# Kernel tuning notes

Measured on AMD Instinct MI355X. Metric: run time of the kernel, lower is better.

Reference implementation:

```python
import jax, jax.numpy as jnp
import numpy as np
from jax import lax

T, IN, H, B = 256, 2048, 2048, 8
K_INIT = 4.0

def setup_inputs() -> dict:
    key = jax.random.key(0)
    k1, k2, k3, k4, k5, k6 = jax.random.split(key, 6)
    k = 1.0 / np.sqrt(H)
    # simplex-init alphas: off-diagonal -K, diagonal log(1-(B-1)exp(-K)), plus small noise
    base = jnp.full((B, B), -K_INIT) + jnp.eye(B) * (np.log(1.0 - (B - 1) * np.exp(-K_INIT)) + K_INIT)
    alphas = base + 0.01 * jax.random.normal(k1, (B, B))
    return {
        "x": jax.random.normal(k2, (T, IN), dtype=jnp.float32),            # sentence of word vectors
        "W": jax.random.uniform(k3, (B, H, H), minval=-k, maxval=k),       # B recurrent basis matrices
        "alphas": alphas.astype(jnp.float32),                               # [B, B] mixing logits
        "bias": jax.random.uniform(k4, (H,), minval=-k, maxval=k),
        "v": jnp.eye(H, IN, dtype=jnp.float32),                             # input projection (init = eye)
        "fc_w": jax.random.uniform(k5, (H, H), minval=-k, maxval=k),
        "fc_b": jax.random.uniform(k6, (H,), minval=-k, maxval=k),
        "alpha_int": 0,
    }

def reference(x, W, alphas, bias, v, fc_w, fc_b, alpha_int):
    # normalise_alpha == softmax over the selected alpha row (simplex=True)
    alpha = jax.nn.softmax(alphas[alpha_int])                 # [B]
    u = jnp.einsum('b,bij->ij', alpha, W)                     # mixed recurrent weight [H, H]
    igates = x @ v.T                                          # all input gates at once [T, H]

    def step(h, ig):                                          # Elman cell: h = tanh(v@w + u@h + bias)
        h = jnp.tanh(ig + u @ h + bias)
        return h, None

    h0 = jnp.zeros((H,), dtype=x.dtype)
    h, _ = lax.scan(step, h0, igates)                         # sequential over T words
    out = jax.nn.sigmoid(h @ fc_w.T + fc_b)                   # fc(hidden.t()) then sigmoid
    return out[None, :]                                       # [1, H]
```

## Files before the change

kernel.cpp:

```cpp
#include <hip/hip_runtime.h>
#include <math.h>

#define NBLK    64
#define NTHR    512
#define HDIM    2048
#define TSTEPS  256
#define BBASIS  8
#define RPB     32
#define RPW     4
#define TTILE   8

typedef float f32x4 __attribute__((ext_vector_type(4)));

__device__ inline void store_coherent_f4(float* p, f32x4 v) {
    asm volatile("global_store_dwordx4 %0, %1, off sc0 sc1"
                 :: "v"(p), "v"(v) : "memory");
}

__device__ inline f32x4 load_coherent_f4(const float* p) {
    f32x4 a;
    asm volatile("global_load_dwordx4 %0, %1, off sc0 sc1\n\t"
                 "s_waitcnt vmcnt(0)"
                 : "=&v"(a) : "v"(p) : "memory");
    return a;
}

__global__ __launch_bounds__(NTHR, 1)
void elman_scan_kernel(const float* __restrict__ x,
                       const float* __restrict__ W,
                       const float* __restrict__ alphas,
                       const float* __restrict__ bias,
                       const float* __restrict__ v,
                       const float* __restrict__ fc_w,
                       const float* __restrict__ fc_b,
                       const int*   __restrict__ alpha_int,
                       float*       __restrict__ out,
                       float*       __restrict__ hbuf)
{
    const int tid  = threadIdx.x;
    const int bid  = blockIdx.x;
    const int wave = tid >> 6;
    const int lane = tid & 63;
    const int r0   = bid * RPB + wave * RPW;

    __shared__ __align__(16) float x_tile[TTILE][HDIM];
    __shared__ __align__(16) float ig_lds[TSTEPS][RPB];
    __shared__ __align__(16) float h_lds[2][HDIM];
    __shared__ __align__(16) float hstage[RPB];

    const int ai = alpha_int[0];
    float a[BBASIS];
    float mx = -1e30f;
    #pragma unroll
    for (int b = 0; b < BBASIS; ++b) { a[b] = alphas[ai * BBASIS + b]; mx = fmaxf(mx, a[b]); }
    float ssum = 0.f;
    #pragma unroll
    for (int b = 0; b < BBASIS; ++b) { a[b] = expf(a[b] - mx); ssum += a[b]; }
    const float inv_s = 1.f / ssum;

    {
        float vr[RPW][8][4];
        #pragma unroll
        for (int q = 0; q < RPW; ++q) {
            const f32x4* vrow = (const f32x4*)(v + (size_t)(r0 + q) * HDIM);
            #pragma unroll
            for (int k = 0; k < 8; ++k) {
                f32x4 t4 = vrow[lane + 64 * k];
                vr[q][k][0] = t4.x; vr[q][k][1] = t4.y; vr[q][k][2] = t4.z; vr[q][k][3] = t4.w;
            }
        }
        for (int tb = 0; tb < TSTEPS; tb += TTILE) {
            #pragma unroll
            for (int j = 0; j < TTILE; ++j)
                *(f32x4*)&x_tile[j][4 * tid] =
                    *(const f32x4*)&x[(size_t)(tb + j) * HDIM + 4 * tid];
            __syncthreads();
            #pragma unroll
            for (int j = 0; j < TTILE; ++j) {
                float acc0 = 0.f, acc1 = 0.f, acc2 = 0.f, acc3 = 0.f;
                #pragma unroll
                for (int k = 0; k < 8; ++k) {
                    const f32x4 x4 = ((const f32x4*)x_tile[j])[lane + 64 * k];
                    acc0 += vr[0][k][0]*x4.x + vr[0][k][1]*x4.y + vr[0][k][2]*x4.z + vr[0][k][3]*x4.w;
                    acc1 += vr[1][k][0]*x4.x + vr[1][k][1]*x4.y + vr[1][k][2]*x4.z + vr[1][k][3]*x4.w;
                    acc2 += vr[2][k][0]*x4.x + vr[2][k][1]*x4.y + vr[2][k][2]*x4.z + vr[2][k][3]*x4.w;
                    acc3 += vr[3][k][0]*x4.x + vr[3][k][1]*x4.y + vr[3][k][2]*x4.z + vr[3][k][3]*x4.w;
                }
                #pragma unroll
                for (int off = 32; off > 0; off >>= 1) {
                    acc0 += __shfl_xor(acc0, off, 64);
                    acc1 += __shfl_xor(acc1, off, 64);
                    acc2 += __shfl_xor(acc2, off, 64);
                    acc3 += __shfl_xor(acc3, off, 64);
                }
                if (lane == 0) {
                    f32x4 ig4; ig4.x = acc0; ig4.y = acc1; ig4.z = acc2; ig4.w = acc3;
                    *(f32x4*)&ig_lds[tb + j][wave * RPW] = ig4;
                }
            }
            __syncthreads();
        }
    }

    float u_reg[RPW][8][4];
    #pragma unroll
    for (int q = 0; q < RPW; ++q)
        #pragma unroll
        for (int k = 0; k < 8; ++k)
            #pragma unroll
            for (int i = 0; i < 4; ++i) u_reg[q][k][i] = 0.f;

    for (int b = 0; b < BBASIS; ++b) {
        const float ab = a[b] * inv_s;
        #pragma unroll
        for (int q = 0; q < RPW; ++q) {
            const f32x4* wrow = (const f32x4*)(W + ((size_t)b * HDIM + (size_t)(r0 + q)) * HDIM);
            #pragma unroll
            for (int k = 0; k < 8; ++k) {
                f32x4 w4 = wrow[lane + 64 * k];
                u_reg[q][k][0] += ab * w4.x;
                u_reg[q][k][1] += ab * w4.y;
                u_reg[q][k][2] += ab * w4.z;
                u_reg[q][k][3] += ab * w4.w;
            }
        }
    }
    float bias4[RPW];
    #pragma unroll
    for (int q = 0; q < RPW; ++q) bias4[q] = bias[r0 + q];

    for (int i = tid; i < HDIM; i += NTHR) h_lds[0][i] = 0.f;
    __syncthreads();

    int cur = 0;
    for (int t = 0; t < TSTEPS; ++t) {
        float acc0 = 0.f, acc1 = 0.f, acc2 = 0.f, acc3 = 0.f;
        #pragma unroll
        for (int k = 0; k < 8; ++k) {
            const f32x4 h4 = ((const f32x4*)h_lds[cur])[lane + 64 * k];
            acc0 += u_reg[0][k][0]*h4.x + u_reg[0][k][1]*h4.y + u_reg[0][k][2]*h4.z + u_reg[0][k][3]*h4.w;
            acc1 += u_reg[1][k][0]*h4.x + u_reg[1][k][1]*h4.y + u_reg[1][k][2]*h4.z + u_reg[1][k][3]*h4.w;
            acc2 += u_reg[2][k][0]*h4.x + u_reg[2][k][1]*h4.y + u_reg[2][k][2]*h4.z + u_reg[2][k][3]*h4.w;
            acc3 += u_reg[3][k][0]*h4.x + u_reg[3][k][1]*h4.y + u_reg[3][k][2]*h4.z + u_reg[3][k][3]*h4.w;
        }
        #pragma unroll
        for (int off = 32; off > 0; off >>= 1) {
            acc0 += __shfl_xor(acc0, off, 64);
            acc1 += __shfl_xor(acc1, off, 64);
            acc2 += __shfl_xor(acc2, off, 64);
            acc3 += __shfl_xor(acc3, off, 64);
        }
        if (lane == 0) {
            const f32x4 ig4 = *(const f32x4*)&ig_lds[t][wave * RPW];
            f32x4 hv;
            hv.x = tanhf(acc0 + ig4.x + bias4[0]);
            hv.y = tanhf(acc1 + ig4.y + bias4[1]);
            hv.z = tanhf(acc2 + ig4.z + bias4[2]);
            hv.w = tanhf(acc3 + ig4.w + bias4[3]);
            *(f32x4*)&hstage[wave * RPW] = hv;
        }
        __syncthreads();

        float* hg = hbuf + (size_t)(t + 1) * HDIM;
        if (wave == 0 && lane < 8) {
            f32x4 hv = *(const f32x4*)&hstage[lane * 4];
            store_coherent_f4(hg + bid * RPB + lane * 4, hv);
        }

        const float* pp = hg + 4 * tid;
        f32x4 hq = load_coherent_f4(pp);
        const unsigned s = 0xFFFFFFFFu;
        while ((__float_as_uint(hq.x) == s) | (__float_as_uint(hq.y) == s) |
               (__float_as_uint(hq.z) == s) | (__float_as_uint(hq.w) == s)) {
            __builtin_amdgcn_s_sleep(2);
            hq = load_coherent_f4(pp);
        }
        const int nxt = cur ^ 1;
        *(f32x4*)&h_lds[nxt][4 * tid] = hq;
        __syncthreads();
        cur = nxt;
    }

    {
        float acc0 = 0.f, acc1 = 0.f, acc2 = 0.f, acc3 = 0.f;
        const f32x4* f0 = (const f32x4*)(fc_w + (size_t)(r0 + 0) * HDIM);
        const f32x4* f1 = (const f32x4*)(fc_w + (size_t)(r0 + 1) * HDIM);
        const f32x4* f2 = (const f32x4*)(fc_w + (size_t)(r0 + 2) * HDIM);
        const f32x4* f3 = (const f32x4*)(fc_w + (size_t)(r0 + 3) * HDIM);
        #pragma unroll
        for (int k = 0; k < 8; ++k) {
            const f32x4 h4 = ((const f32x4*)h_lds[cur])[lane + 64 * k];
            f32x4 w0 = f0[lane + 64 * k];
            f32x4 w1 = f1[lane + 64 * k];
            f32x4 w2 = f2[lane + 64 * k];
            f32x4 w3 = f3[lane + 64 * k];
            acc0 += w0.x*h4.x + w0.y*h4.y + w0.z*h4.z + w0.w*h4.w;
            acc1 += w1.x*h4.x + w1.y*h4.y + w1.z*h4.z + w1.w*h4.w;
            acc2 += w2.x*h4.x + w2.y*h4.y + w2.z*h4.z + w2.w*h4.w;
            acc3 += w3.x*h4.x + w3.y*h4.y + w3.z*h4.z + w3.w*h4.w;
        }
        #pragma unroll
        for (int off = 32; off > 0; off >>= 1) {
            acc0 += __shfl_xor(acc0, off, 64);
            acc1 += __shfl_xor(acc1, off, 64);
            acc2 += __shfl_xor(acc2, off, 64);
            acc3 += __shfl_xor(acc3, off, 64);
        }
        if (lane == 0) {
            f32x4 o4;
            o4.x = 1.f / (1.f + expf(-(acc0 + fc_b[r0 + 0])));
            o4.y = 1.f / (1.f + expf(-(acc1 + fc_b[r0 + 1])));
            o4.z = 1.f / (1.f + expf(-(acc2 + fc_b[r0 + 2])));
            o4.w = 1.f / (1.f + expf(-(acc3 + fc_b[r0 + 3])));
            *(f32x4*)&out[r0] = o4;
        }
    }
}

extern "C" void kernel_launch(void* const* d_in, const int* in_sizes, int n_in,
                              void* d_out, int out_size, void* d_ws, size_t ws_size,
                              hipStream_t stream)
{
    const float* x      = (const float*)d_in[0];
    const float* W      = (const float*)d_in[1];
    const float* alphas = (const float*)d_in[2];
    const float* bias   = (const float*)d_in[3];
    const float* v      = (const float*)d_in[4];
    const float* fc_w   = (const float*)d_in[5];
    const float* fc_b   = (const float*)d_in[6];
    const int*   ai     = (const int*)d_in[7];
    float* out = (float*)d_out;

    float* hbuf = (float*)d_ws;
    const size_t hbuf_bytes = (size_t)(TSTEPS + 1) * HDIM * sizeof(float);

    hipMemsetAsync(d_ws, 0xFF, hbuf_bytes, stream);

    elman_scan_kernel<<<NBLK, NTHR, 0, stream>>>(x, W, alphas, bias, v, fc_w, fc_b,
                                                 ai, out, hbuf);
}
```

Baseline: 1.043 ms.

## Split prep (mixed weights, input gates) into wide kernel before persistent scan

Moves the basis mixing of W and the x@v.T input-gate projection into a separate prep kernel launched on 256 blocks, writing u and igates to workspace. The persistent 64-block scan kernel then only loads them. This spreads the setup work across more CUs than the 64 used by the scan. The scan step also drops the LDS staging and extra barrier: each wave's lane 0 stores its 4 h values directly, and the spin sleep is shortened. The cost is an extra kernel launch and a global round-trip for u and igates. The original single kernel remains as a fallback when the workspace is too small.

```diff
diff --git a/kernel.cpp b/kernel.cpp
--- a/kernel.cpp
+++ b/kernel.cpp
@@ -1,14 +1,9 @@
 #include <hip/hip_runtime.h>
 #include <math.h>
 
-#define NBLK    64
-#define NTHR    512
 #define HDIM    2048
 #define TSTEPS  256
 #define BBASIS  8
-#define RPB     32
-#define RPW     4
-#define TTILE   8
 
 typedef float f32x4 __attribute__((ext_vector_type(4)));
 
@@ -16,7 +11,6 @@
     asm volatile("global_store_dwordx4 %0, %1, off sc0 sc1"
                  :: "v"(p), "v"(v) : "memory");
 }
-
 __device__ inline f32x4 load_coherent_f4(const float* p) {
     f32x4 a;
     asm volatile("global_load_dwordx4 %0, %1, off sc0 sc1\n\t"
@@ -25,28 +19,22 @@
     return a;
 }
 
-__global__ __launch_bounds__(NTHR, 1)
-void elman_scan_kernel(const float* __restrict__ x,
-                       const float* __restrict__ W,
-                       const float* __restrict__ alphas,
-                       const float* __restrict__ bias,
-                       const float* __restrict__ v,
-                       const float* __restrict__ fc_w,
-                       const float* __restrict__ fc_b,
-                       const int*   __restrict__ alpha_int,
-                       float*       __restrict__ out,
-                       float*       __restrict__ hbuf)
+__global__ __launch_bounds__(256, 1)
+void prep_kernel(const float* __restrict__ x,
+                 const float* __restrict__ W,
+                 const float* __restrict__ alphas,
+                 const float* __restrict__ v,
+                 const int*   __restrict__ alpha_int,
+                 float*       __restrict__ u_g,
+                 float*       __restrict__ ig_g)
 {
     const int tid  = threadIdx.x;
     const int bid  = blockIdx.x;
     const int wave = tid >> 6;
     const int lane = tid & 63;
-    const int r0   = bid * RPB + wave * RPW;
-
-    __shared__ __align__(16) float x_tile[TTILE][HDIM];
-    __shared__ __align__(16) float ig_lds[TSTEPS][RPB];
-    __shared__ __align__(16) float h_lds[2][HDIM];
-    __shared__ __align__(16) float hstage[RPB];
+    const int r0   = bid * 8 + wave * 2;
+
+    __shared__ __align__(16) float x_tile[8][HDIM];
 
     const int ai = alpha_int[0];
     float a[BBASIS];
@@ -59,9 +47,46 @@
     const float inv_s = 1.f / ssum;
 
     {
-        float vr[RPW][8][4];
-        #pragma unroll
-        for (int q = 0; q < RPW; ++q) {
+        float acc[2][8][4];
+        #pragma unroll
+        for (int q = 0; q < 2; ++q)
+            #pragma unroll
+            for (int k = 0; k < 8; ++k)
+                #pragma unroll
+                for (int i = 0; i < 4; ++i) acc[q][k][i] = 0.f;
+
+        for (int b = 0; b < BBASIS; ++b) {
+            const float ab = a[b] * inv_s;
+            #pragma unroll
+            for (int q = 0; q < 2; ++q) {
+                const f32x4* wrow = (const f32x4*)(W + ((size_t)b * HDIM + (size_t)(r0 + q)) * HDIM);
+                #pragma unroll
+                for (int k = 0; k < 8; ++k) {
+                    f32x4 w4 = wrow[lane + 64 * k];
+                    acc[q][k][0] += ab * w4.x;
+                    acc[q][k][1] += ab * w4.y;
+                    acc[q][k][2] += ab * w4.z;
+                    acc[q][k][3] += ab * w4.w;
+                }
+            }
+        }
+        #pragma unroll
+        for (int q = 0; q < 2; ++q) {
+            f32x4* urow = (f32x4*)(u_g + (size_t)(r0 + q) * HDIM);
+            #pragma unroll
+            for (int k = 0; k < 8; ++k) {
+                f32x4 w4;
+                w4.x = acc[q][k][0]; w4.y = acc[q][k][1];
+                w4.z = acc[q][k][2]; w4.w = acc[q][k][3];
+                urow[lane + 64 * k] = w4;
+            }
+        }
+    }
+
+    {
+        float vr[2][8][4];
+        #pragma unroll
+        for (int q = 0; q < 2; ++q) {
             const f32x4* vrow = (const f32x4*)(v + (size_t)(r0 + q) * HDIM);
             #pragma unroll
             for (int k = 0; k < 8; ++k) {
@@ -69,14 +94,214 @@
                 vr[q][k][0] = t4.x; vr[q][k][1] = t4.y; vr[q][k][2] = t4.z; vr[q][k][3] = t4.w;
             }
         }
-        for (int tb = 0; tb < TSTEPS; tb += TTILE) {
-            #pragma unroll
-            for (int j = 0; j < TTILE; ++j)
+        for (int tb = 0; tb < TSTEPS; tb += 8) {
+            #pragma unroll
+            for (int j = 0; j < 8; ++j) {
+                const f32x4* xt4 = (const f32x4*)(x + (size_t)(tb + j) * HDIM);
+                #pragma unroll
+                for (int c = 0; c < 2; ++c)
+                    ((f32x4*)x_tile[j])[tid + 256 * c] = xt4[tid + 256 * c];
+            }
+            __syncthreads();
+            #pragma unroll
+            for (int j = 0; j < 8; ++j) {
+                float acc0 = 0.f, acc1 = 0.f;
+                #pragma unroll
+                for (int k = 0; k < 8; ++k) {
+                    const f32x4 x4 = ((const f32x4*)x_tile[j])[lane + 64 * k];
+                    acc0 += vr[0][k][0]*x4.x + vr[0][k][1]*x4.y + vr[0][k][2]*x4.z + vr[0][k][3]*x4.w;
+                    acc1 += vr[1][k][0]*x4.x + vr[1][k][1]*x4.y + vr[1][k][2]*x4.z + vr[1][k][3]*x4.w;
+                }
+                #pragma unroll
+                for (int off = 32; off > 0; off >>= 1) {
+                    acc0 += __shfl_xor(acc0, off, 64);
+                    acc1 += __shfl_xor(acc1, off, 64);
+                }
+                if (lane == 0)
+                    *(float2*)&ig_g[(size_t)(tb + j) * HDIM + r0] = make_float2(acc0, acc1);
+            }
+            __syncthreads();
+        }
+    }
+}
+
+__global__ __launch_bounds__(512, 1)
+void scan_kernel(const float* __restrict__ bias,
+                 const float* __restrict__ fc_w,
+                 const float* __restrict__ fc_b,
+                 float*       __restrict__ out,
+                 const float* __restrict__ u_g,
+                 const float* __restrict__ ig_g,
+                 float*       __restrict__ hbuf)
+{
+    const int tid  = threadIdx.x;
+    const int bid  = blockIdx.x;
+    const int wave = tid >> 6;
+    const int lane = tid & 63;
+    const int r0   = bid * 32 + wave * 4;
+
+    __shared__ __align__(16) float h_lds[2][HDIM];
+    __shared__ __align__(16) float ig_lds[TSTEPS][32];
+
+    #pragma unroll
+    for (int i = 0; i < 4; ++i) {
+        const int c  = tid + 512 * i;
+        const int t  = c >> 3;
+        const int ch = c & 7;
+        f32x4 g = *(const f32x4*)&ig_g[(size_t)t * HDIM + bid * 32 + ch * 4];
+        *(f32x4*)&ig_lds[t][ch * 4] = g;
+    }
+
+    float u_reg[4][8][4];
+    #pragma unroll
+    for (int q = 0; q < 4; ++q) {
+        const f32x4* urow = (const f32x4*)(u_g + (size_t)(r0 + q) * HDIM);
+        #pragma unroll
+        for (int k = 0; k < 8; ++k) {
+            f32x4 w4 = urow[lane + 64 * k];
+            u_reg[q][k][0] = w4.x; u_reg[q][k][1] = w4.y;
+            u_reg[q][k][2] = w4.z; u_reg[q][k][3] = w4.w;
+        }
+    }
+    float bias4[4];
+    #pragma unroll
+    for (int q = 0; q < 4; ++q) bias4[q] = bias[r0 + q];
+
+    h_lds[0][tid]        = 0.f;
+    h_lds[0][tid + 512]  = 0.f;
+    h_lds[0][tid + 1024] = 0.f;
+    h_lds[0][tid + 1536] = 0.f;
+    __syncthreads();
+
+    int cur = 0;
+    for (int t = 0; t < TSTEPS; ++t) {
+        float acc0 = 0.f, acc1 = 0.f, acc2 = 0.f, acc3 = 0.f;
+        #pragma unroll
+        for (int k = 0; k < 8; ++k) {
+            const f32x4 h4 = ((const f32x4*)h_lds[cur])[lane + 64 * k];
+            acc0 += u_reg[0][k][0]*h4.x + u_reg[0][k][1]*h4.y + u_reg[0][k][2]*h4.z + u_reg[0][k][3]*h4.w;
+            acc1 += u_reg[1][k][0]*h4.x + u_reg[1][k][1]*h4.y + u_reg[1][k][2]*h4.z + u_reg[1][k][3]*h4.w;
+            acc2 += u_reg[2][k][0]*h4.x + u_reg[2][k][1]*h4.y + u_reg[2][k][2]*h4.z + u_reg[2][k][3]*h4.w;
+            acc3 += u_reg[3][k][0]*h4.x + u_reg[3][k][1]*h4.y + u_reg[3][k][2]*h4.z + u_reg[3][k][3]*h4.w;
+        }
+        #pragma unroll
+        for (int off = 32; off > 0; off >>= 1) {
+            acc0 += __shfl_xor(acc0, off, 64);
+            acc1 += __shfl_xor(acc1, off, 64);
+            acc2 += __shfl_xor(acc2, off, 64);
+            acc3 += __shfl_xor(acc3, off, 64);
+        }
+        float* hg = hbuf + (size_t)(t + 1) * HDIM;
+        if (lane == 0) {
+            const f32x4 ig4 = *(const f32x4*)&ig_lds[t][wave * 4];
+            f32x4 hv;
+            hv.x = tanhf(acc0 + ig4.x + bias4[0]);
+            hv.y = tanhf(acc1 + ig4.y + bias4[1]);
+            hv.z = tanhf(acc2 + ig4.z + bias4[2]);
+            hv.w = tanhf(acc3 + ig4.w + bias4[3]);
+            store_coherent_f4(hg + r0, hv);
+        }
+        const float* pp = hg + 4 * tid;
+        f32x4 hq = load_coherent_f4(pp);
+        const unsigned s = 0xFFFFFFFFu;
+        while ((__float_as_uint(hq.x) == s) | (__float_as_uint(hq.y) == s) |
+               (__float_as_uint(hq.z) == s) | (__float_as_uint(hq.w) == s)) {
+            __builtin_amdgcn_s_sleep(1);
+            hq = load_coherent_f4(pp);
+        }
+        const int nxt = cur ^ 1;
+        *(f32x4*)&h_lds[nxt][4 * tid] = hq;
+        __syncthreads();
+        cur = nxt;
+    }
+
+    {
+        float acc0 = 0.f, acc1 = 0.f, acc2 = 0.f, acc3 = 0.f;
+        const f32x4* f0 = (const f32x4*)(fc_w + (size_t)(r0 + 0) * HDIM);
+        const f32x4* f1 = (const f32x4*)(fc_w + (size_t)(r0 + 1) * HDIM);
+        const f32x4* f2 = (const f32x4*)(fc_w + (size_t)(r0 + 2) * HDIM);
+        const f32x4* f3 = (const f32x4*)(fc_w + (size_t)(r0 + 3) * HDIM);
+        #pragma unroll
+        for (int k = 0; k < 8; ++k) {
+            const f32x4 h4 = ((const f32x4*)h_lds[cur])[lane + 64 * k];
+            f32x4 w0 = f0[lane + 64 * k];
+            f32x4 w1 = f1[lane + 64 * k];
+            f32x4 w2 = f2[lane + 64 * k];
+            f32x4 w3 = f3[lane + 64 * k];
+            acc0 += w0.x*h4.x + w0.y*h4.y + w0.z*h4.z + w0.w*h4.w;
+            acc1 += w1.x*h4.x + w1.y*h4.y + w1.z*h4.z + w1.w*h4.w;
+            acc2 += w2.x*h4.x + w2.y*h4.y + w2.z*h4.z + w2.w*h4.w;
+            acc3 += w3.x*h4.x + w3.y*h4.y + w3.z*h4.z + w3.w*h4.w;
+        }
+        #pragma unroll
+        for (int off = 32; off > 0; off >>= 1) {
+            acc0 += __shfl_xor(acc0, off, 64);
+            acc1 += __shfl_xor(acc1, off, 64);
+            acc2 += __shfl_xor(acc2, off, 64);
+            acc3 += __shfl_xor(acc3, off, 64);
+        }
+        if (lane == 0) {
+            f32x4 o4;
+            o4.x = 1.f / (1.f + expf(-(acc0 + fc_b[r0 + 0])));
+            o4.y = 1.f / (1.f + expf(-(acc1 + fc_b[r0 + 1])));
+            o4.z = 1.f / (1.f + expf(-(acc2 + fc_b[r0 + 2])));
+            o4.w = 1.f / (1.f + expf(-(acc3 + fc_b[r0 + 3])));
+            *(f32x4*)&out[r0] = o4;
+        }
+    }
+}
+
+__global__ __launch_bounds__(512, 1)
+void elman_scan_self(const float* __restrict__ x,
+                     const float* __restrict__ W,
+                     const float* __restrict__ alphas,
+                     const float* __restrict__ bias,
+                     const float* __restrict__ v,
+                     const float* __restrict__ fc_w,
+                     const float* __restrict__ fc_b,
+                     const int*   __restrict__ alpha_int,
+                     float*       __restrict__ out,
+                     float*       __restrict__ hbuf)
+{
+    const int tid  = threadIdx.x;
+    const int bid  = blockIdx.x;
+    const int wave = tid >> 6;
+    const int lane = tid & 63;
+    const int r0   = bid * 32 + wave * 4;
+
+    __shared__ __align__(16) float x_tile[8][HDIM];
+    __shared__ __align__(16) float ig_lds[TSTEPS][32];
+    __shared__ __align__(16) float h_lds[2][HDIM];
+
+    const int ai = alpha_int[0];
+    float a[BBASIS];
+    float mx = -1e30f;
+    #pragma unroll
+    for (int b = 0; b < BBASIS; ++b) { a[b] = alphas[ai * BBASIS + b]; mx = fmaxf(mx, a[b]); }
+    float ssum = 0.f;
+    #pragma unroll
+    for (int b = 0; b < BBASIS; ++b) { a[b] = expf(a[b] - mx); ssum += a[b]; }
+    const float inv_s = 1.f / ssum;
+
+    {
+        float vr[4][8][4];
+        #pragma unroll
+        for (int q = 0; q < 4; ++q) {
+            const f32x4* vrow = (const f32x4*)(v + (size_t)(r0 + q) * HDIM);
+            #pragma unroll
+            for (int k = 0; k < 8; ++k) {
+                f32x4 t4 = vrow[lane + 64 * k];
+                vr[q][k][0] = t4.x; vr[q][k][1] = t4.y; vr[q][k][2] = t4.z; vr[q][k][3] = t4.w;
+            }
+        }
+        for (int tb = 0; tb < TSTEPS; tb += 8) {
+            #pragma unroll
+            for (int j = 0; j < 8; ++j)
                 *(f32x4*)&x_tile[j][4 * tid] =
                     *(const f32x4*)&x[(size_t)(tb + j) * HDIM + 4 * tid];
             __syncthreads();
             #pragma unroll
-            for (int j = 0; j < TTILE; ++j) {
+            for (int j = 0; j < 8; ++j) {
                 float acc0 = 0.f, acc1 = 0.f, acc2 = 0.f, acc3 = 0.f;
                 #pragma unroll
                 for (int k = 0; k < 8; ++k) {
@@ -95,16 +320,16 @@
                 }
                 if (lane == 0) {
                     f32x4 ig4; ig4.x = acc0; ig4.y = acc1; ig4.z = acc2; ig4.w = acc3;
-                    *(f32x4*)&ig_lds[tb + j][wave * RPW] = ig4;
+                    *(f32x4*)&ig_lds[tb + j][wave * 4] = ig4;
                 }
             }
             __syncthreads();
         }
     }
 
-    float u_reg[RPW][8][4];
-    #pragma unroll
-    for (int q = 0; q < RPW; ++q)
+    float u_reg[4][8][4];
+    #pragma unroll
+    for (int q = 0; q < 4; ++q)
         #pragma unroll
         for (int k = 0; k < 8; ++k)
             #pragma unroll
@@ -113,7 +338,7 @@
     for (int b = 0; b < BBASIS; ++b) {
         const float ab = a[b] * inv_s;
         #pragma unroll
-        for (int q = 0; q < RPW; ++q) {
+        for (int q = 0; q < 4; ++q) {
             const f32x4* wrow = (const f32x4*)(W + ((size_t)b * HDIM + (size_t)(r0 + q)) * HDIM);
             #pragma unroll
             for (int k = 0; k < 8; ++k) {
@@ -125,11 +350,12 @@
             }
         }
     }
-    float bias4[RPW];
-    #pragma unroll
-    for (int q = 0; q < RPW; ++q) bias4[q] = bias[r0 + q];
-
-    for (int i = tid; i < HDIM; i += NTHR) h_lds[0][i] = 0.f;
+    float bias4[4];
+    #pragma unroll
+    for (int q = 0; q < 4; ++q) bias4[q] = bias[r0 + q];
+
+    h_lds[0][tid] = 0.f; h_lds[0][tid + 512] = 0.f;
+    h_lds[0][tid + 1024] = 0.f; h_lds[0][tid + 1536] = 0.f;
     __syncthreads();
 
     int cur = 0;
@@ -150,29 +376,22 @@
             acc2 += __shfl_xor(acc2, off, 64);
             acc3 += __shfl_xor(acc3, off, 64);
         }
+        float* hg = hbuf + (size_t)(t + 1) * HDIM;
         if (lane == 0) {
-            const f32x4 ig4 = *(const f32x4*)&ig_lds[t][wave * RPW];
+            const f32x4 ig4 = *(const f32x4*)&ig_lds[t][wave * 4];
             f32x4 hv;
             hv.x = tanhf(acc0 + ig4.x + bias4[0]);
             hv.y = tanhf(acc1 + ig4.y + bias4[1]);
             hv.z = tanhf(acc2 + ig4.z + bias4[2]);
             hv.w = tanhf(acc3 + ig4.w + bias4[3]);
-            *(f32x4*)&hstage[wave * RPW] = hv;
-        }
-        __syncthreads();
-
-        float* hg = hbuf + (size_t)(t + 1) * HDIM;
-        if (wave == 0 && lane < 8) {
-            f32x4 hv = *(const f32x4*)&hstage[lane * 4];
-            store_coherent_f4(hg + bid * RPB + lane * 4, hv);
-        }
-
+            store_coherent_f4(hg + r0, hv);
+        }
         const float* pp = hg + 4 * tid;
         f32x4 hq = load_coherent_f4(pp);
         const unsigned s = 0xFFFFFFFFu;
         while ((__float_as_uint(hq.x) == s) | (__float_as_uint(hq.y) == s) |
                (__float_as_uint(hq.z) == s) | (__float_as_uint(hq.w) == s)) {
-            __builtin_amdgcn_s_sleep(2);
+            __builtin_amdgcn_s_sleep(1);
             hq = load_coherent_f4(pp);
         }
         const int nxt = cur ^ 1;
@@ -231,11 +450,24 @@
     const int*   ai     = (const int*)d_in[7];
     float* out = (float*)d_out;
 
+    const size_t HB_BYTES = (size_t)(TSTEPS + 1) * HDIM * sizeof(float);
+    const size_t IG_OFF   = 0x210000;
+    const size_t IG_BYTES = (size_t)TSTEPS * HDIM * sizeof(float);
+    const size_t U_OFF    = IG_OFF + 0x210000;
+    const size_t U_BYTES  = (size_t)HDIM * HDIM * sizeof(float);
+    const size_t NEED     = U_OFF + U_BYTES;
+
     float* hbuf = (float*)d_ws;
-    const size_t hbuf_bytes = (size_t)(TSTEPS + 1) * HDIM * sizeof(float);
-
-    hipMemsetAsync(d_ws, 0xFF, hbuf_bytes, stream);
-
-    elman_scan_kernel<<<NBLK, NTHR, 0, stream>>>(x, W, alphas, bias, v, fc_w, fc_b,
-                                                 ai, out, hbuf);
-}
+
+    hipMemsetAsync(d_ws, 0xFF, HB_BYTES, stream);
+
+    if (ws_size >= NEED) {
+        float* ig_g = (float*)((char*)d_ws + IG_OFF);
+        float* u_g  = (float*)((char*)d_ws + U_OFF);
+        prep_kernel<<<256, 256, 0, stream>>>(x, W, alphas, v, ai, u_g, ig_g);
+        scan_kernel<<<64, 512, 0, stream>>>(bias, fc_w, fc_b, out, u_g, ig_g, hbuf);
+    } else {
+        elman_scan_self<<<64, 512, 0, stream>>>(x, W, alphas, bias, v, fc_w, fc_b,
+                                                ai, out, hbuf);
+    }
+}
```

Result: no change. 1.033 ms (-0.9%).
